# Kernel tuning notes

Measured on AMD Instinct MI355X. Metric: run time of the kernel, lower is better.

Reference implementation:

```python
import jax, jax.numpy as jnp
import numpy as np

B, N, NS, D, HID, MH = 256, 4096, 8, 64, 128, 128
ITERS, EPS, SCALE = 3, 1e-8, D ** -0.5

def _ln(x, g, b):
    m = jnp.mean(x, -1, keepdims=True)
    v = jnp.var(x, -1, keepdims=True)
    return (x - m) * jax.lax.rsqrt(v + 1e-5) * g + b

def _mlp2(x, W1, b1, W2, b2):
    return jax.nn.relu(x @ W1.T + b1) @ W2.T + b2

def _gru(x, h, Wih, Whh, bih, bhh):
    gi = x @ Wih.T + bih
    gh = h @ Whh.T + bhh
    ir, iz, inn = jnp.split(gi, 3, -1)
    hr, hz, hn = jnp.split(gh, 3, -1)
    r = jax.nn.sigmoid(ir + hr)
    z = jax.nn.sigmoid(iz + hz)
    n = jnp.tanh(inn + r * hn)
    return (1 - z) * n + z * h

def _kl(post, prior):
    # KL(N(m_po, exp(lv_po)) || N(m_pr, exp(lv_pr))), diagonal Gaussians, per row
    m_po, lv_po = post[:, :D], post[:, D:]
    m_pr, lv_pr = prior[:, :D], prior[:, D:]
    return 0.5 * jnp.sum(lv_pr - lv_po + (jnp.exp(lv_po) + (m_po - m_pr) ** 2) * jnp.exp(-lv_pr) - 1.0, -1)

def _fwd(inputs, slots, prior_slots, eps_noise, ni_g, ni_b, npf_g, npf_b, Wq, bq, Wk, bk, Wv, bv, sr_W1, sr_b1, sr_W2, sr_b2, pr_W1, pr_b1, pr_W2, pr_b2, gru_Wih, gru_Whh, gru_bih, gru_bhh, mlp_W1, mlp_b1, mlp_W2, mlp_b2):
    b = inputs.shape[0]
    x = _ln(inputs, ni_g, ni_b)               # [b,n,d]
    k = x @ Wk.T + bk
    v = x @ Wv.T + bv
    prior = _mlp2(jax.lax.stop_gradient(prior_slots).reshape(-1, D), pr_W1, pr_b1, pr_W2, pr_b2)  # [b*ns,2d]
    sms = _mlp2(slots.reshape(-1, D), sr_W1, sr_b1, sr_W2, sr_b2).reshape(b, NS, 2 * D)
    mu, logvar = sms[:, :, :D], sms[:, :, D:]
    slots = eps_noise * jnp.exp(0.5 * logvar) + mu   # reparameterize
    kl = jnp.zeros((b * NS,), inputs.dtype)
    for _ in range(ITERS):
        slots_prev = slots
        q = slots @ Wq.T + bq
        dots = jnp.einsum('bid,bjd->bij', q, k) * SCALE   # [b,ns,n]
        attn = jax.nn.softmax(dots, axis=1) + EPS          # softmax over SLOTS (dim=1)
        attn = attn / jnp.sum(attn, -1, keepdims=True)     # renormalize over inputs
        updates = jnp.einsum('bjd,bij->bid', v, attn)      # [b,ns,d]
        slots = _gru(updates.reshape(-1, D), slots_prev.reshape(-1, D), gru_Wih, gru_Whh, gru_bih, gru_bhh).reshape(b, NS, D)
        slots = slots + _mlp2(_ln(slots, npf_g, npf_b), mlp_W1, mlp_b1, mlp_W2, mlp_b2)
        post = _mlp2(slots.reshape(-1, D), sr_W1, sr_b1, sr_W2, sr_b2)
        kl = kl + _kl(post, prior)
    return slots, kl

def setup_inputs() -> dict:
    key = jax.random.key(0)
    ks = jax.random.split(key, 16)
    f32 = jnp.float32
    def w(k, shape):
        return (jax.random.normal(k, shape) * 0.02).astype(f32)
    return {
        'inputs': jax.random.normal(ks[0], (B, N, D), f32),
        'slots': jax.random.normal(ks[1], (B, NS, D), f32),
        'prior_slots': jax.random.normal(ks[2], (B, NS, D), f32),
        'eps_noise': jax.random.normal(ks[3], (B, NS, D), f32),
        'ni_g': jnp.ones((D,), f32), 'ni_b': jnp.zeros((D,), f32),
        'npf_g': jnp.ones((D,), f32), 'npf_b': jnp.zeros((D,), f32),
        'Wq': w(ks[4], (D, D)), 'bq': jnp.zeros((D,), f32),
        'Wk': w(ks[5], (D, D)), 'bk': jnp.zeros((D,), f32),
        'Wv': w(ks[6], (D, D)), 'bv': jnp.zeros((D,), f32),
        'sr_W1': w(ks[7], (HID, D)), 'sr_b1': jnp.zeros((HID,), f32),
        'sr_W2': w(ks[8], (2 * D, HID)), 'sr_b2': jnp.zeros((2 * D,), f32),
        'pr_W1': w(ks[9], (HID, D)), 'pr_b1': jnp.zeros((HID,), f32),
        'pr_W2': w(ks[10], (2 * D, HID)), 'pr_b2': jnp.zeros((2 * D,), f32),
        'gru_Wih': w(ks[11], (3 * D, D)), 'gru_Whh': w(ks[12], (3 * D, D)),
        'gru_bih': jnp.zeros((3 * D,), f32), 'gru_bhh': jnp.zeros((3 * D,), f32),
        'mlp_W1': w(ks[13], (MH, D)), 'mlp_b1': jnp.zeros((MH,), f32),
        'mlp_W2': w(ks[14], (D, MH)), 'mlp_b2': jnp.zeros((D,), f32),
    }

def reference(inputs, slots, prior_slots, eps_noise, ni_g, ni_b, npf_g, npf_b, Wq, bq, Wk, bk, Wv, bv, sr_W1, sr_b1, sr_W2, sr_b2, pr_W1, pr_b1, pr_W2, pr_b2, gru_Wih, gru_Whh, gru_bih, gru_bhh, mlp_W1, mlp_b1, mlp_W2, mlp_b2):
    return _fwd(inputs, slots, prior_slots, eps_noise, ni_g, ni_b, npf_g, npf_b, Wq, bq, Wk, bk, Wv, bv, sr_W1, sr_b1, sr_W2, sr_b2, pr_W1, pr_b1, pr_W2, pr_b2, gru_Wih, gru_Whh, gru_bih, gru_bhh, mlp_W1, mlp_b1, mlp_W2, mlp_b2)
```

## Files before the change

### kernel.cpp

```cpp
#include <hip/hip_runtime.h>
#include <cstdint>
#include <cstddef>


#define B_   256
#define N_   4096
#define EPS_   1e-8f
#define SCALE_ 0.125f
#define OUT_SLOTS_ (B_ * 8 * 64)

typedef unsigned short u16;
typedef unsigned int   u32;
typedef short s16x8 __attribute__((ext_vector_type(8)));
typedef float f32x4 __attribute__((ext_vector_type(4)));

__device__ inline float bf2f(u16 u) {
  union { u32 i; float f; } c; c.i = ((u32)u) << 16; return c.f;
}
__device__ inline u16 f2bf(float f) {
  union { u32 i; float f; } c; c.f = f;
  return (u16)((c.i + 0x7fffu + ((c.i >> 16) & 1u)) >> 16);
}
__device__ inline void bf2x2(u32 u, float& lo, float& hi) {
  union { u32 i; float f; } a, b;
  a.i = u << 16; b.i = u & 0xffff0000u;
  lo = a.f; hi = b.f;
}
__device__ inline float wredsum(float v) {
  #pragma unroll
  for (int o = 32; o; o >>= 1) v += __shfl_xor(v, o, 64);
  return v;
}
__device__ inline float dot64(const float* __restrict__ x, const float* __restrict__ w, float a) {
  #pragma unroll
  for (int ec = 0; ec < 16; ec++) {
    float4 xe = ((const float4*)x)[ec]; float4 we = ((const float4*)w)[ec];
    a = fmaf(xe.x, we.x, a); a = fmaf(xe.y, we.y, a);
    a = fmaf(xe.z, we.z, a); a = fmaf(xe.w, we.w, a);
  }
  return a;
}
__device__ inline float dot128(const float* __restrict__ x, const float* __restrict__ w, float a) {
  #pragma unroll
  for (int ec = 0; ec < 32; ec++) {
    float4 xe = ((const float4*)x)[ec]; float4 we = ((const float4*)w)[ec];
    a = fmaf(xe.x, we.x, a); a = fmaf(xe.y, we.y, a);
    a = fmaf(xe.z, we.z, a); a = fmaf(xe.w, we.w, a);
  }
  return a;
}

__global__ __launch_bounds__(256) void k_ln(
    const float* __restrict__ x, const float* __restrict__ gg,
    const float* __restrict__ bb, u16* __restrict__ XH)
{
  const int tid = threadIdx.x;
  const int xc = tid & 3;
  const int rloc = tid >> 2;
  float4 g4[4], b4[4];
  #pragma unroll
  for (int j = 0; j < 4; j++) {
    g4[j] = *(const float4*)(gg + xc * 16 + j * 4);
    b4[j] = *(const float4*)(bb + xc * 16 + j * 4);
  }
  for (size_t base = (size_t)blockIdx.x * 64; base < (size_t)B_ * N_;
       base += (size_t)gridDim.x * 64) {
    const size_t row = base + rloc;
    const float* xr = x + row * 64 + xc * 16;
    float4 xv[4];
    #pragma unroll
    for (int j = 0; j < 4; j++) xv[j] = ((const float4*)xr)[j];
    float s = 0.f;
    #pragma unroll
    for (int j = 0; j < 4; j++) s += xv[j].x + xv[j].y + xv[j].z + xv[j].w;
    s += __shfl_xor(s, 1, 64); s += __shfl_xor(s, 2, 64);
    const float m = s * (1.0f / 64.0f);
    float vs = 0.f;
    #pragma unroll
    for (int j = 0; j < 4; j++) {
      float a0 = xv[j].x - m, a1 = xv[j].y - m, a2 = xv[j].z - m, a3 = xv[j].w - m;
      vs += a0*a0 + a1*a1 + a2*a2 + a3*a3;
    }
    vs += __shfl_xor(vs, 1, 64); vs += __shfl_xor(vs, 2, 64);
    const float rs = rsqrtf(vs * (1.0f / 64.0f) + 1e-5f);
    u32 pk[8];
    #pragma unroll
    for (int j = 0; j < 4; j++) {
      float h0 = (xv[j].x - m) * rs * g4[j].x + b4[j].x;
      float h1 = (xv[j].y - m) * rs * g4[j].y + b4[j].y;
      float h2 = (xv[j].z - m) * rs * g4[j].z + b4[j].z;
      float h3 = (xv[j].w - m) * rs * g4[j].w + b4[j].w;
      pk[j*2+0] = (u32)f2bf(h0) | ((u32)f2bf(h1) << 16);
      pk[j*2+1] = (u32)f2bf(h2) | ((u32)f2bf(h3) << 16);
    }
    u32* dst = (u32*)(XH + row * 64 + xc * 16);
    ((uint4*)dst)[0] = make_uint4(pk[0], pk[1], pk[2], pk[3]);
    ((uint4*)dst)[1] = make_uint4(pk[4], pk[5], pk[6], pk[7]);
  }
}

__global__ __launch_bounds__(256) void k_setup(
    const float* __restrict__ gWih, const float* __restrict__ gbih,
    const float* __restrict__ Wv,   const float* __restrict__ bv,
    const float* __restrict__ Wq,   const float* __restrict__ bq,
    const float* __restrict__ Wk,   const float* __restrict__ bk,
    float* __restrict__ WF, float* __restrict__ bF,
    float* __restrict__ WQKs, float* __restrict__ bQKs,
    float* __restrict__ wcs, float* __restrict__ c0s)
{
  const int gid = blockIdx.x * 256 + threadIdx.x;
  if (gid < 12288) {
    int r = gid >> 6, e = gid & 63;
    float a = 0.f;
    #pragma unroll 8
    for (int d = 0; d < 64; d++) a = fmaf(gWih[r*64+d], Wv[d*64+e], a);
    WF[gid] = a;
  } else if (gid < 16384) {
    int o = gid - 12288; int t = o >> 6, e = o & 63;
    float a = 0.f;
    #pragma unroll 8
    for (int d = 0; d < 64; d++) a = fmaf(Wq[d*64+t], Wk[d*64+e], a);
    WQKs[o] = a * SCALE_;
  } else if (gid < 16576) {
    int r = gid - 16384;
    float a = gbih[r];
    #pragma unroll 8
    for (int d = 0; d < 64; d++) a = fmaf(gWih[r*64+d], bv[d], a);
    bF[r] = a;
  } else if (gid < 16640) {
    int e = gid - 16576;
    float a = 0.f;
    #pragma unroll 8
    for (int d = 0; d < 64; d++) a = fmaf(bq[d], Wk[d*64+e], a);
    bQKs[e] = a * SCALE_;
  } else if (gid < 16704) {
    int t = gid - 16640;
    float a = 0.f;
    #pragma unroll 8
    for (int d = 0; d < 64; d++) a = fmaf(Wq[d*64+t], bk[d], a);
    wcs[t] = a * SCALE_;
  } else if (gid == 16704) {
    float a = 0.f;
    #pragma unroll 8
    for (int d = 0; d < 64; d++) a = fmaf(bq[d], bk[d], a);
    c0s[0] = a * SCALE_;
  }
}

__global__ __launch_bounds__(256) void k_init(
    const float* __restrict__ slots0, const float* __restrict__ prior_slots,
    const float* __restrict__ eps_noise,
    const float* __restrict__ sr_W1, const float* __restrict__ sr_b1,
    const float* __restrict__ sr_W2, const float* __restrict__ sr_b2,
    const float* __restrict__ pr_W1, const float* __restrict__ pr_b1,
    const float* __restrict__ pr_W2, const float* __restrict__ pr_b2,
    const float* __restrict__ WQKs, const float* __restrict__ bQKs,
    const float* __restrict__ wcs, const float* __restrict__ c0s,
    float* __restrict__ SLOTS, float* __restrict__ PRIOR, float* __restrict__ KLb,
    u16* __restrict__ QP, float* __restrict__ Cb)
{
  __shared__ float sl[256], hid[512], pst[512];
  const int tid = threadIdx.x;
  const int w = tid >> 6, lane = tid & 63;
  const int gs0 = blockIdx.x * 4;
  const int b = gs0 >> 3;
  const int gs = gs0 + w;

  sl[tid] = slots0[(size_t)gs0 * 64 + tid];
  #pragma unroll
  for (int kk = 0; kk < 2; kk++) {
    int idx = tid + kk * 256; int sloc = idx >> 7, h = idx & 127;
    float a = dot64(prior_slots + (size_t)(gs0 + sloc) * 64, pr_W1 + h * 64, pr_b1[h]);
    hid[idx] = fmaxf(a, 0.f);
  }
  __syncthreads();
  #pragma unroll
  for (int kk = 0; kk < 2; kk++) {
    int idx = tid + kk * 256; int sloc = idx >> 7, o = idx & 127;
    PRIOR[(size_t)(gs0 + sloc) * 128 + o] =
        dot128(hid + sloc * 128, pr_W2 + o * 128, pr_b2[o]);
  }
  __syncthreads();
  #pragma unroll
  for (int kk = 0; kk < 2; kk++) {
    int idx = tid + kk * 256; int sloc = idx >> 7, h = idx & 127;
    float a = dot64(sl + sloc * 64, sr_W1 + h * 64, sr_b1[h]);
    hid[idx] = fmaxf(a, 0.f);
  }
  __syncthreads();
  #pragma unroll
  for (int kk = 0; kk < 2; kk++) {
    int idx = tid + kk * 256; int sloc = idx >> 7, o = idx & 127;
    pst[idx] = dot128(hid + sloc * 128, sr_W2 + o * 128, sr_b2[o]);
  }
  __syncthreads();
  {
    float mu = pst[w * 128 + lane];
    float lv = pst[w * 128 + 64 + lane];
    float sv = eps_noise[(size_t)gs * 64 + lane] * __expf(0.5f * lv) + mu;
    sl[tid] = sv;
    SLOTS[(size_t)gs * 64 + lane] = sv;
  }
  __syncthreads();
  {
    float a = bQKs[lane];
    #pragma unroll 8
    for (int t2 = 0; t2 < 64; t2++) a = fmaf(sl[w * 64 + t2], WQKs[t2 * 64 + lane], a);
    QP[(size_t)b * 1024 + (gs & 7) * 64 + lane] = f2bf(a);
    float part = wredsum(sl[tid] * wcs[lane]);
    if (lane == 0) { Cb[b * 16 + (gs & 7)] = part + c0s[0]; KLb[gs] = 0.f; }
    QP[(size_t)b * 1024 + 512 + (blockIdx.x & 1) * 256 + tid] = 0;
    if ((blockIdx.x & 1) == 0 && tid < 8) Cb[b * 16 + 8 + tid] = 0.f;
  }
}

__global__ __launch_bounds__(256, 4) void k_attn(
    const u16* __restrict__ XH, const u16* __restrict__ QP,
    const float* __restrict__ Cb,
    float* __restrict__ Upart, float* __restrict__ Spart)
{
  __shared__ float attn[8][516];
  __shared__ float updw[4][512];
  __shared__ float sS[4][8];
  const int tid  = threadIdx.x;
  const int lane = tid & 63, wv = tid >> 6;
  const int col  = lane & 15, kg = lane >> 4;
  const int bc   = blockIdx.x;
  const int b    = bc >> 3;
  const u16* Xb = XH + (size_t)bc * 512 * 64;

  union { uint4 q; s16x8 v; } a0, a1;
  const u16* qr = QP + (size_t)b * 1024 + col * 64 + kg * 8;
  a0.q = *(const uint4*)(qr);
  a1.q = *(const uint4*)(qr + 32);
  float4 cv = *(const float4*)(Cb + b * 16 + kg * 4);

  const int jb = wv * 128;
  float s_loc[4] = {0.f, 0.f, 0.f, 0.f};
  union { uint4 q; s16x8 v; } b0, b1, n0, n1;
  {
    const u16* kp = Xb + (size_t)(jb + col) * 64 + kg * 8;
    b0.q = *(const uint4*)kp; b1.q = *(const uint4*)(kp + 32);
  }
  #pragma unroll 1
  for (int t = 0; t < 8; t++) {
    const u16* kn = Xb + (size_t)(jb + (((t + 1) & 7) << 4) + col) * 64 + kg * 8;
    n0.q = *(const uint4*)kn; n1.q = *(const uint4*)(kn + 32);
    f32x4 acc = {0.f, 0.f, 0.f, 0.f};
    acc = __builtin_amdgcn_mfma_f32_16x16x32_bf16(a0.v, b0.v, acc, 0, 0, 0);
    acc = __builtin_amdgcn_mfma_f32_16x16x32_bf16(a1.v, b1.v, acc, 0, 0, 0);
    float d0 = acc[0] + cv.x, d1 = acc[1] + cv.y;
    float d2 = acc[2] + cv.z, d3 = acc[3] + cv.w;
    float m4 = fmaxf(fmaxf(d0, d1), fmaxf(d2, d3));
    float m8 = fmaxf(m4, __shfl_xor(m4, 16, 64));
    float e0 = __expf(d0 - m8), e1 = __expf(d1 - m8);
    float e2 = __expf(d2 - m8), e3 = __expf(d3 - m8);
    float s4 = e0 + e1 + e2 + e3;
    float s8 = s4 + __shfl_xor(s4, 16, 64);
    float rinv = 1.0f / s8;
    float v0 = fmaf(e0, rinv, EPS_), v1 = fmaf(e1, rinv, EPS_);
    float v2 = fmaf(e2, rinv, EPS_), v3 = fmaf(e3, rinv, EPS_);
    if (kg < 2) {
      int j = jb + t * 16 + col;
      attn[kg*4+0][j] = v0; attn[kg*4+1][j] = v1;
      attn[kg*4+2][j] = v2; attn[kg*4+3][j] = v3;
      s_loc[0] += v0; s_loc[1] += v1; s_loc[2] += v2; s_loc[3] += v3;
    }
    b0 = n0; b1 = n1;
  }
  #pragma unroll
  for (int r = 0; r < 4; r++) {
    #pragma unroll
    for (int o = 1; o < 16; o <<= 1) s_loc[r] += __shfl_xor(s_loc[r], o, 64);
  }
  if (kg < 2 && col == 0) {
    #pragma unroll
    for (int r = 0; r < 4; r++) sS[wv][kg * 4 + r] = s_loc[r];
  }

  const int pxo  = lane >> 4;
  const int dimc = lane & 15;
  float u[8][4];
  #pragma unroll
  for (int i = 0; i < 8; i++)
    #pragma unroll
    for (int dd = 0; dd < 4; dd++) u[i][dd] = 0.f;
  #pragma unroll 4
  for (int jg = 0; jg < 32; jg++) {
    int j = jb + jg * 4 + pxo;
    uint2 xv2 = *(const uint2*)(Xb + (size_t)j * 64 + dimc * 4);
    float x0, x1, x2, x3;
    bf2x2(xv2.x, x0, x1); bf2x2(xv2.y, x2, x3);
    #pragma unroll
    for (int i = 0; i < 8; i++) {
      float a = attn[i][j];
      u[i][0] = fmaf(a, x0, u[i][0]); u[i][1] = fmaf(a, x1, u[i][1]);
      u[i][2] = fmaf(a, x2, u[i][2]); u[i][3] = fmaf(a, x3, u[i][3]);
    }
  }
  #pragma unroll
  for (int i = 0; i < 8; i++)
    #pragma unroll
    for (int dd = 0; dd < 4; dd++) {
      u[i][dd] += __shfl_xor(u[i][dd], 16, 64);
      u[i][dd] += __shfl_xor(u[i][dd], 32, 64);
    }
  if (lane < 16) {
    #pragma unroll
    for (int i = 0; i < 8; i++)
      #pragma unroll
      for (int dd = 0; dd < 4; dd++)
        updw[wv][i * 64 + lane * 4 + dd] = u[i][dd];
  }
  __syncthreads();
  #pragma unroll
  for (int k2 = 0; k2 < 2; k2++) {
    int idx = tid + k2 * 256;
    Upart[(size_t)bc * 512 + idx] =
        updw[0][idx] + updw[1][idx] + updw[2][idx] + updw[3][idx];
  }
  if (tid < 8)
    Spart[bc * 8 + tid] = sS[0][tid] + sS[1][tid] + sS[2][tid] + sS[3][tid];
}

__global__ __launch_bounds__(256) void k_update(
    float* __restrict__ SLOTS, const float* __restrict__ Upart,
    const float* __restrict__ Spart, const float* __restrict__ PRIOR,
    float* __restrict__ KLb, u16* __restrict__ QP, float* __restrict__ Cb,
    const float* __restrict__ npf_g, const float* __restrict__ npf_b,
    const float* __restrict__ WF, const float* __restrict__ bF,
    const float* __restrict__ gWhh, const float* __restrict__ gbhh,
    const float* __restrict__ WQKs, const float* __restrict__ bQKs,
    const float* __restrict__ wcs, const float* __restrict__ c0s,
    const float* __restrict__ sr_W1, const float* __restrict__ sr_b1,
    const float* __restrict__ sr_W2, const float* __restrict__ sr_b2,
    const float* __restrict__ mW1, const float* __restrict__ mb1,
    const float* __restrict__ mW2, const float* __restrict__ mb2,
    float* __restrict__ out, int last)
{
  __shared__ float uav[256], spl[256], sl[256], lnb[256], hid[512], pst[512];
  const int tid = threadIdx.x;
  const int w = tid >> 6, lane = tid & 63;
  const int gs = blockIdx.x * 4 + w;
  const int b = gs >> 3, s = gs & 7;

  {
    const float* up = Upart + (size_t)b * 4096 + s * 64 + lane;
    float usum = 0.f;
    #pragma unroll
    for (int c = 0; c < 8; c++) usum += up[c * 512];
    const float* sp2 = Spart + b * 64 + s;
    float Sv = 0.f;
    #pragma unroll
    for (int c = 0; c < 8; c++) Sv += sp2[c * 8];
    uav[tid] = usum * (1.0f / Sv);
    spl[tid] = SLOTS[(size_t)gs * 64 + lane];
  }
  __syncthreads();
  {
    const float* ur = uav + w * 64;
    const float* hr = spl + w * 64;
    const float* wi0 = WF + lane * 64;
    const float* wi1 = WF + (64 + lane) * 64;
    const float* wi2 = WF + (128 + lane) * 64;
    const float* wh0 = gWhh + lane * 64;
    const float* wh1 = gWhh + (64 + lane) * 64;
    const float* wh2 = gWhh + (128 + lane) * 64;
    float air = 0.f, aiz = 0.f, ain = 0.f, ahr = 0.f, ahz = 0.f, ahn = 0.f;
    #pragma unroll
    for (int ec = 0; ec < 16; ec++) {
      float4 xe = ((const float4*)ur)[ec];
      float4 he = ((const float4*)hr)[ec];
      float4 ww;
      ww = ((const float4*)wi0)[ec];
      air = fmaf(xe.x,ww.x,air); air = fmaf(xe.y,ww.y,air);
      air = fmaf(xe.z,ww.z,air); air = fmaf(xe.w,ww.w,air);
      ww = ((const float4*)wi1)[ec];
      aiz = fmaf(xe.x,ww.x,aiz); aiz = fmaf(xe.y,ww.y,aiz);
      aiz = fmaf(xe.z,ww.z,aiz); aiz = fmaf(xe.w,ww.w,aiz);
      ww = ((const float4*)wi2)[ec];
      ain = fmaf(xe.x,ww.x,ain); ain = fmaf(xe.y,ww.y,ain);
      ain = fmaf(xe.z,ww.z,ain); ain = fmaf(xe.w,ww.w,ain);
      ww = ((const float4*)wh0)[ec];
      ahr = fmaf(he.x,ww.x,ahr); ahr = fmaf(he.y,ww.y,ahr);
      ahr = fmaf(he.z,ww.z,ahr); ahr = fmaf(he.w,ww.w,ahr);
      ww = ((const float4*)wh1)[ec];
      ahz = fmaf(he.x,ww.x,ahz); ahz = fmaf(he.y,ww.y,ahz);
      ahz = fmaf(he.z,ww.z,ahz); ahz = fmaf(he.w,ww.w,ahz);
      ww = ((const float4*)wh2)[ec];
      ahn = fmaf(he.x,ww.x,ahn); ahn = fmaf(he.y,ww.y,ahn);
      ahn = fmaf(he.z,ww.z,ahn); ahn = fmaf(he.w,ww.w,ahn);
    }
    float rr = 1.0f / (1.0f + __expf(-(air + bF[lane]       + ahr + gbhh[lane])));
    float zz = 1.0f / (1.0f + __expf(-(aiz + bF[64 + lane]  + ahz + gbhh[64 + lane])));
    float nn = tanhf(ain + bF[128 + lane] + rr * (ahn + gbhh[128 + lane]));
    float hnew = (1.0f - zz) * nn + zz * spl[tid];
    sl[tid] = hnew;
    float mm = wredsum(hnew) * (1.0f / 64.0f);
    float cc = hnew - mm;
    float va = wredsum(cc * cc) * (1.0f / 64.0f);
    lnb[tid] = cc * rsqrtf(va + 1e-5f) * npf_g[lane] + npf_b[lane];
  }
  __syncthreads();
  #pragma unroll
  for (int kk = 0; kk < 2; kk++) {
    int idx = tid + kk * 256; int sloc = idx >> 7, h = idx & 127;
    float a = dot64(lnb + sloc * 64, mW1 + h * 64, mb1[h]);
    hid[idx] = fmaxf(a, 0.f);
  }
  __syncthreads();
  sl[tid] += dot128(hid + w * 128, mW2 + lane * 128, mb2[lane]);
  __syncthreads();
  #pragma unroll
  for (int kk = 0; kk < 2; kk++) {
    int idx = tid + kk * 256; int sloc = idx >> 7, h = idx & 127;
    float a = dot64(sl + sloc * 64, sr_W1 + h * 64, sr_b1[h]);
    hid[idx] = fmaxf(a, 0.f);
  }
  __syncthreads();
  #pragma unroll
  for (int kk = 0; kk < 2; kk++) {
    int idx = tid + kk * 256; int sloc = idx >> 7, o = idx & 127;
    pst[idx] = dot128(hid + sloc * 128, sr_W2 + o * 128, sr_b2[o]);
  }
  __syncthreads();
  {
    float m_po = pst[w * 128 + lane],  lv_po = pst[w * 128 + 64 + lane];
    float m_pr = PRIOR[(size_t)gs * 128 + lane];
    float lv_pr = PRIOR[(size_t)gs * 128 + 64 + lane];
    float dm = m_po - m_pr;
    float term = lv_pr - lv_po + (__expf(lv_po) + dm * dm) * __expf(-lv_pr) - 1.0f;
    float tsum = wredsum(term);
    if (lane == 0) {
      float k2 = KLb[gs] + 0.5f * tsum;
      KLb[gs] = k2;
      if (last) out[OUT_SLOTS_ + gs] = k2;
    }
    if (last) {
      out[(size_t)gs * 64 + lane] = sl[tid];
    } else {
      SLOTS[(size_t)gs * 64 + lane] = sl[tid];
      float a = bQKs[lane];
      #pragma unroll 8
      for (int t2 = 0; t2 < 64; t2++) a = fmaf(sl[w * 64 + t2], WQKs[t2 * 64 + lane], a);
      QP[(size_t)b * 1024 + s * 64 + lane] = f2bf(a);
      float part = wredsum(sl[tid] * wcs[lane]);
      if (lane == 0) Cb[b * 16 + s] = part + c0s[0];
    }
  }
}

extern "C" void kernel_launch(void* const* d_in, const int* in_sizes, int n_in,
                              void* d_out, int out_size, void* d_ws, size_t ws_size,
                              hipStream_t stream) {
  (void)in_sizes; (void)n_in; (void)out_size; (void)ws_size;
  const float* inputs      = (const float*)d_in[0];
  const float* slots0      = (const float*)d_in[1];
  const float* prior_slots = (const float*)d_in[2];
  const float* eps_noise   = (const float*)d_in[3];
  const float* ni_g  = (const float*)d_in[4];
  const float* ni_b  = (const float*)d_in[5];
  const float* npf_g = (const float*)d_in[6];
  const float* npf_b = (const float*)d_in[7];
  const float* Wq = (const float*)d_in[8];   const float* bq = (const float*)d_in[9];
  const float* Wk = (const float*)d_in[10];  const float* bk = (const float*)d_in[11];
  const float* Wv = (const float*)d_in[12];  const float* bv = (const float*)d_in[13];
  const float* sr_W1 = (const float*)d_in[14]; const float* sr_b1 = (const float*)d_in[15];
  const float* sr_W2 = (const float*)d_in[16]; const float* sr_b2 = (const float*)d_in[17];
  const float* pr_W1 = (const float*)d_in[18]; const float* pr_b1 = (const float*)d_in[19];
  const float* pr_W2 = (const float*)d_in[20]; const float* pr_b2 = (const float*)d_in[21];
  const float* gWih = (const float*)d_in[22]; const float* gWhh = (const float*)d_in[23];
  const float* gbih = (const float*)d_in[24]; const float* gbhh = (const float*)d_in[25];
  const float* mW1 = (const float*)d_in[26]; const float* mb1 = (const float*)d_in[27];
  const float* mW2 = (const float*)d_in[28]; const float* mb2 = (const float*)d_in[29];

  char* ws = (char*)d_ws;
  u16*   XH    = (u16*)  (ws);
  float* Upart = (float*)(ws + 134217728);
  float* Spart = (float*)(ws + 138412032);
  u16*   QP    = (u16*)  (ws + 138477568);
  float* Cb    = (float*)(ws + 139001856);
  float* SLOTS = (float*)(ws + 139018240);
  float* PRIOR = (float*)(ws + 139542528);
  float* KLb   = (float*)(ws + 140591104);
  float* WF    = (float*)(ws + 140599296);
  float* WQKs  = (float*)(ws + 140648448);
  float* bF    = (float*)(ws + 140664832);
  float* bQKs  = (float*)(ws + 140665600);
  float* wcs   = (float*)(ws + 140665856);
  float* c0s   = (float*)(ws + 140666112);

  k_setup<<<dim3(66), dim3(256), 0, stream>>>(
      gWih, gbih, Wv, bv, Wq, bq, Wk, bk, WF, bF, WQKs, bQKs, wcs, c0s);
  k_ln<<<dim3(4096), dim3(256), 0, stream>>>(inputs, ni_g, ni_b, XH);
  k_init<<<dim3(512), dim3(256), 0, stream>>>(
      slots0, prior_slots, eps_noise,
      sr_W1, sr_b1, sr_W2, sr_b2, pr_W1, pr_b1, pr_W2, pr_b2,
      WQKs, bQKs, wcs, c0s, SLOTS, PRIOR, KLb, QP, Cb);
  for (int it = 0; it < 3; it++) {
    k_attn<<<dim3(2048), dim3(256), 0, stream>>>(XH, QP, Cb, Upart, Spart);
    k_update<<<dim3(512), dim3(256), 0, stream>>>(
        SLOTS, Upart, Spart, PRIOR, KLb, QP, Cb,
        npf_g, npf_b, WF, bF, gWhh, gbhh, WQKs, bQKs, wcs, c0s,
        sr_W1, sr_b1, sr_W2, sr_b2, mW1, mb1, mW2, mb2,
        (float*)d_out, it == 2);
  }
}
```

Baseline: 768.2 us.

## Fuse setup kernels into one launch and use MFMA for attention-value product

Merges the layernorm, weight-precompute and slot-init kernels into a single launch partitioned by block index. The init path now computes q explicitly and projects it through Wk instead of reading precomputed WQKs, so it no longer depends on the fused precompute blocks. In the attention kernel, the scalar FMA loop that multiplied attention weights by bf16 inputs is replaced with bf16 MFMA: attention weights and input tiles are staged through LDS per 32-pixel group. The update kernel switches to per-wave LDS slices and redistributes MLP work per wave. The MFMA path rounds attention weights to bf16, adds per-group block syncs and uses strided LDS reads for the B operand.

```diff
diff --git a/kernel.cpp b/kernel.cpp
--- a/kernel.cpp
+++ b/kernel.cpp
@@ -14,17 +14,9 @@
 typedef short s16x8 __attribute__((ext_vector_type(8)));
 typedef float f32x4 __attribute__((ext_vector_type(4)));
 
-__device__ inline float bf2f(u16 u) {
-  union { u32 i; float f; } c; c.i = ((u32)u) << 16; return c.f;
-}
 __device__ inline u16 f2bf(float f) {
   union { u32 i; float f; } c; c.f = f;
   return (u16)((c.i + 0x7fffu + ((c.i >> 16) & 1u)) >> 16);
-}
-__device__ inline void bf2x2(u32 u, float& lo, float& hi) {
-  union { u32 i; float f; } a, b;
-  a.i = u << 16; b.i = u & 0xffff0000u;
-  lo = a.f; hi = b.f;
 }
 __device__ inline float wredsum(float v) {
   #pragma unroll
@@ -50,167 +42,150 @@
   return a;
 }
 
-__global__ __launch_bounds__(256) void k_ln(
+__global__ __launch_bounds__(256) void k_pre(
     const float* __restrict__ x, const float* __restrict__ gg,
-    const float* __restrict__ bb, u16* __restrict__ XH)
-{
-  const int tid = threadIdx.x;
-  const int xc = tid & 3;
-  const int rloc = tid >> 2;
-  float4 g4[4], b4[4];
-  #pragma unroll
-  for (int j = 0; j < 4; j++) {
-    g4[j] = *(const float4*)(gg + xc * 16 + j * 4);
-    b4[j] = *(const float4*)(bb + xc * 16 + j * 4);
-  }
-  for (size_t base = (size_t)blockIdx.x * 64; base < (size_t)B_ * N_;
-       base += (size_t)gridDim.x * 64) {
-    const size_t row = base + rloc;
-    const float* xr = x + row * 64 + xc * 16;
-    float4 xv[4];
-    #pragma unroll
-    for (int j = 0; j < 4; j++) xv[j] = ((const float4*)xr)[j];
-    float s = 0.f;
-    #pragma unroll
-    for (int j = 0; j < 4; j++) s += xv[j].x + xv[j].y + xv[j].z + xv[j].w;
-    s += __shfl_xor(s, 1, 64); s += __shfl_xor(s, 2, 64);
-    const float m = s * (1.0f / 64.0f);
-    float vs = 0.f;
-    #pragma unroll
-    for (int j = 0; j < 4; j++) {
-      float a0 = xv[j].x - m, a1 = xv[j].y - m, a2 = xv[j].z - m, a3 = xv[j].w - m;
-      vs += a0*a0 + a1*a1 + a2*a2 + a3*a3;
-    }
-    vs += __shfl_xor(vs, 1, 64); vs += __shfl_xor(vs, 2, 64);
-    const float rs = rsqrtf(vs * (1.0f / 64.0f) + 1e-5f);
-    u32 pk[8];
-    #pragma unroll
-    for (int j = 0; j < 4; j++) {
-      float h0 = (xv[j].x - m) * rs * g4[j].x + b4[j].x;
-      float h1 = (xv[j].y - m) * rs * g4[j].y + b4[j].y;
-      float h2 = (xv[j].z - m) * rs * g4[j].z + b4[j].z;
-      float h3 = (xv[j].w - m) * rs * g4[j].w + b4[j].w;
-      pk[j*2+0] = (u32)f2bf(h0) | ((u32)f2bf(h1) << 16);
-      pk[j*2+1] = (u32)f2bf(h2) | ((u32)f2bf(h3) << 16);
-    }
-    u32* dst = (u32*)(XH + row * 64 + xc * 16);
-    ((uint4*)dst)[0] = make_uint4(pk[0], pk[1], pk[2], pk[3]);
-    ((uint4*)dst)[1] = make_uint4(pk[4], pk[5], pk[6], pk[7]);
-  }
-}
-
-__global__ __launch_bounds__(256) void k_setup(
-    const float* __restrict__ gWih, const float* __restrict__ gbih,
-    const float* __restrict__ Wv,   const float* __restrict__ bv,
-    const float* __restrict__ Wq,   const float* __restrict__ bq,
-    const float* __restrict__ Wk,   const float* __restrict__ bk,
-    float* __restrict__ WF, float* __restrict__ bF,
-    float* __restrict__ WQKs, float* __restrict__ bQKs,
-    float* __restrict__ wcs, float* __restrict__ c0s)
-{
-  const int gid = blockIdx.x * 256 + threadIdx.x;
-  if (gid < 12288) {
-    int r = gid >> 6, e = gid & 63;
-    float a = 0.f;
-    #pragma unroll 8
-    for (int d = 0; d < 64; d++) a = fmaf(gWih[r*64+d], Wv[d*64+e], a);
-    WF[gid] = a;
-  } else if (gid < 16384) {
-    int o = gid - 12288; int t = o >> 6, e = o & 63;
-    float a = 0.f;
-    #pragma unroll 8
-    for (int d = 0; d < 64; d++) a = fmaf(Wq[d*64+t], Wk[d*64+e], a);
-    WQKs[o] = a * SCALE_;
-  } else if (gid < 16576) {
-    int r = gid - 16384;
-    float a = gbih[r];
-    #pragma unroll 8
-    for (int d = 0; d < 64; d++) a = fmaf(gWih[r*64+d], bv[d], a);
-    bF[r] = a;
-  } else if (gid < 16640) {
-    int e = gid - 16576;
-    float a = 0.f;
-    #pragma unroll 8
-    for (int d = 0; d < 64; d++) a = fmaf(bq[d], Wk[d*64+e], a);
-    bQKs[e] = a * SCALE_;
-  } else if (gid < 16704) {
-    int t = gid - 16640;
-    float a = 0.f;
-    #pragma unroll 8
-    for (int d = 0; d < 64; d++) a = fmaf(Wq[d*64+t], bk[d], a);
-    wcs[t] = a * SCALE_;
-  } else if (gid == 16704) {
-    float a = 0.f;
-    #pragma unroll 8
-    for (int d = 0; d < 64; d++) a = fmaf(bq[d], bk[d], a);
-    c0s[0] = a * SCALE_;
-  }
-}
-
-__global__ __launch_bounds__(256) void k_init(
+    const float* __restrict__ bb, u16* __restrict__ XH,
     const float* __restrict__ slots0, const float* __restrict__ prior_slots,
     const float* __restrict__ eps_noise,
     const float* __restrict__ sr_W1, const float* __restrict__ sr_b1,
     const float* __restrict__ sr_W2, const float* __restrict__ sr_b2,
     const float* __restrict__ pr_W1, const float* __restrict__ pr_b1,
     const float* __restrict__ pr_W2, const float* __restrict__ pr_b2,
-    const float* __restrict__ WQKs, const float* __restrict__ bQKs,
-    const float* __restrict__ wcs, const float* __restrict__ c0s,
+    const float* __restrict__ Wq,   const float* __restrict__ bq,
+    const float* __restrict__ Wk,   const float* __restrict__ bk,
+    const float* __restrict__ gWih, const float* __restrict__ gbih,
+    const float* __restrict__ Wv,   const float* __restrict__ bv,
     float* __restrict__ SLOTS, float* __restrict__ PRIOR, float* __restrict__ KLb,
-    u16* __restrict__ QP, float* __restrict__ Cb)
+    u16* __restrict__ QP, float* __restrict__ Cb,
+    float* __restrict__ WF, float* __restrict__ bF,
+    float* __restrict__ WQKs, float* __restrict__ bQKs,
+    float* __restrict__ wcs, float* __restrict__ c0s)
 {
-  __shared__ float sl[256], hid[512], pst[512];
+  __shared__ float ism[4][256];
   const int tid = threadIdx.x;
-  const int w = tid >> 6, lane = tid & 63;
-  const int gs0 = blockIdx.x * 4;
-  const int b = gs0 >> 3;
-  const int gs = gs0 + w;
-
-  sl[tid] = slots0[(size_t)gs0 * 64 + tid];
-  #pragma unroll
-  for (int kk = 0; kk < 2; kk++) {
-    int idx = tid + kk * 256; int sloc = idx >> 7, h = idx & 127;
-    float a = dot64(prior_slots + (size_t)(gs0 + sloc) * 64, pr_W1 + h * 64, pr_b1[h]);
-    hid[idx] = fmaxf(a, 0.f);
-  }
-  __syncthreads();
-  #pragma unroll
-  for (int kk = 0; kk < 2; kk++) {
-    int idx = tid + kk * 256; int sloc = idx >> 7, o = idx & 127;
-    PRIOR[(size_t)(gs0 + sloc) * 128 + o] =
-        dot128(hid + sloc * 128, pr_W2 + o * 128, pr_b2[o]);
-  }
-  __syncthreads();
-  #pragma unroll
-  for (int kk = 0; kk < 2; kk++) {
-    int idx = tid + kk * 256; int sloc = idx >> 7, h = idx & 127;
-    float a = dot64(sl + sloc * 64, sr_W1 + h * 64, sr_b1[h]);
-    hid[idx] = fmaxf(a, 0.f);
-  }
-  __syncthreads();
-  #pragma unroll
-  for (int kk = 0; kk < 2; kk++) {
-    int idx = tid + kk * 256; int sloc = idx >> 7, o = idx & 127;
-    pst[idx] = dot128(hid + sloc * 128, sr_W2 + o * 128, sr_b2[o]);
-  }
-  __syncthreads();
-  {
-    float mu = pst[w * 128 + lane];
-    float lv = pst[w * 128 + 64 + lane];
+  const int bid = blockIdx.x;
+
+  if (bid < 4096) {
+    const int xc = tid & 3;
+    const int rloc = tid >> 2;
+    float4 g4[4], b4[4];
+    #pragma unroll
+    for (int j = 0; j < 4; j++) {
+      g4[j] = *(const float4*)(gg + xc * 16 + j * 4);
+      b4[j] = *(const float4*)(bb + xc * 16 + j * 4);
+    }
+    for (int it = 0; it < 4; it++) {
+      const size_t row = ((size_t)bid + (size_t)it * 4096) * 64 + rloc;
+      const float* xr = x + row * 64 + xc * 16;
+      float4 xv[4];
+      #pragma unroll
+      for (int j = 0; j < 4; j++) xv[j] = ((const float4*)xr)[j];
+      float s = 0.f;
+      #pragma unroll
+      for (int j = 0; j < 4; j++) s += xv[j].x + xv[j].y + xv[j].z + xv[j].w;
+      s += __shfl_xor(s, 1, 64); s += __shfl_xor(s, 2, 64);
+      const float m = s * (1.0f / 64.0f);
+      float vs = 0.f;
+      #pragma unroll
+      for (int j = 0; j < 4; j++) {
+        float a0 = xv[j].x - m, a1 = xv[j].y - m, a2 = xv[j].z - m, a3 = xv[j].w - m;
+        vs += a0*a0 + a1*a1 + a2*a2 + a3*a3;
+      }
+      vs += __shfl_xor(vs, 1, 64); vs += __shfl_xor(vs, 2, 64);
+      const float rs = rsqrtf(vs * (1.0f / 64.0f) + 1e-5f);
+      u32 pk[8];
+      #pragma unroll
+      for (int j = 0; j < 4; j++) {
+        float h0 = (xv[j].x - m) * rs * g4[j].x + b4[j].x;
+        float h1 = (xv[j].y - m) * rs * g4[j].y + b4[j].y;
+        float h2 = (xv[j].z - m) * rs * g4[j].z + b4[j].z;
+        float h3 = (xv[j].w - m) * rs * g4[j].w + b4[j].w;
+        pk[j*2+0] = (u32)f2bf(h0) | ((u32)f2bf(h1) << 16);
+        pk[j*2+1] = (u32)f2bf(h2) | ((u32)f2bf(h3) << 16);
+      }
+      u32* dst = (u32*)(XH + row * 64 + xc * 16);
+      ((uint4*)dst)[0] = make_uint4(pk[0], pk[1], pk[2], pk[3]);
+      ((uint4*)dst)[1] = make_uint4(pk[4], pk[5], pk[6], pk[7]);
+    }
+  } else if (bid < 4608) {
+    const int ib = bid - 4096;
+    const int w = tid >> 6, lane = tid & 63;
+    const int gs = ib * 4 + w;
+    const int b  = gs >> 3;
+    float* slL  = ism[w];
+    float* hidL = ism[w] + 64;
+    float* qL   = ism[w] + 192;
+
+    slL[lane] = slots0[(size_t)gs * 64 + lane];
+    const float* prow = prior_slots + (size_t)gs * 64;
+    float ph0 = dot64(prow, pr_W1 + lane * 64,        pr_b1[lane]);
+    float ph1 = dot64(prow, pr_W1 + (64 + lane) * 64, pr_b1[64 + lane]);
+    hidL[lane]      = fmaxf(ph0, 0.f);
+    hidL[64 + lane] = fmaxf(ph1, 0.f);
+    __syncthreads();
+    PRIOR[(size_t)gs * 128 + lane]      = dot128(hidL, pr_W2 + lane * 128,        pr_b2[lane]);
+    PRIOR[(size_t)gs * 128 + 64 + lane] = dot128(hidL, pr_W2 + (64 + lane) * 128, pr_b2[64 + lane]);
+    __syncthreads();
+    float sh0 = dot64(slL, sr_W1 + lane * 64,        sr_b1[lane]);
+    float sh1 = dot64(slL, sr_W1 + (64 + lane) * 64, sr_b1[64 + lane]);
+    hidL[lane]      = fmaxf(sh0, 0.f);
+    hidL[64 + lane] = fmaxf(sh1, 0.f);
+    __syncthreads();
+    float mu = dot128(hidL, sr_W2 + lane * 128,        sr_b2[lane]);
+    float lv = dot128(hidL, sr_W2 + (64 + lane) * 128, sr_b2[64 + lane]);
     float sv = eps_noise[(size_t)gs * 64 + lane] * __expf(0.5f * lv) + mu;
-    sl[tid] = sv;
     SLOTS[(size_t)gs * 64 + lane] = sv;
-  }
-  __syncthreads();
-  {
-    float a = bQKs[lane];
+    slL[lane] = sv;
+    __syncthreads();
+    float q = dot64(slL, Wq + lane * 64, bq[lane]);
+    qL[lane] = q;
+    __syncthreads();
+    float qp = 0.f;
     #pragma unroll 8
-    for (int t2 = 0; t2 < 64; t2++) a = fmaf(sl[w * 64 + t2], WQKs[t2 * 64 + lane], a);
-    QP[(size_t)b * 1024 + (gs & 7) * 64 + lane] = f2bf(a);
-    float part = wredsum(sl[tid] * wcs[lane]);
-    if (lane == 0) { Cb[b * 16 + (gs & 7)] = part + c0s[0]; KLb[gs] = 0.f; }
-    QP[(size_t)b * 1024 + 512 + (blockIdx.x & 1) * 256 + tid] = 0;
-    if ((blockIdx.x & 1) == 0 && tid < 8) Cb[b * 16 + 8 + tid] = 0.f;
+    for (int t2 = 0; t2 < 64; t2++) qp = fmaf(qL[t2], Wk[t2 * 64 + lane], qp);
+    QP[(size_t)b * 1024 + (gs & 7) * 64 + lane] = f2bf(qp * SCALE_);
+    float c = wredsum(q * bk[lane]) * SCALE_;
+    if (lane == 0) { Cb[b * 16 + (gs & 7)] = c; KLb[gs] = 0.f; }
+    QP[(size_t)b * 1024 + 512 + (ib & 1) * 256 + tid] = 0;
+    if ((ib & 1) == 0 && tid < 8) Cb[b * 16 + 8 + tid] = 0.f;
+  } else {
+    const int gid = (bid - 4608) * 256 + tid;
+    if (gid < 12288) {
+      int r = gid >> 6, e = gid & 63;
+      float a = 0.f;
+      #pragma unroll 8
+      for (int d = 0; d < 64; d++) a = fmaf(gWih[r*64+d], Wv[d*64+e], a);
+      WF[gid] = a;
+    } else if (gid < 16384) {
+      int o = gid - 12288; int t = o >> 6, e = o & 63;
+      float a = 0.f;
+      #pragma unroll 8
+      for (int d = 0; d < 64; d++) a = fmaf(Wq[d*64+t], Wk[d*64+e], a);
+      WQKs[o] = a * SCALE_;
+    } else if (gid < 16576) {
+      int r = gid - 16384;
+      float a = gbih[r];
+      #pragma unroll 8
+      for (int d = 0; d < 64; d++) a = fmaf(gWih[r*64+d], bv[d], a);
+      bF[r] = a;
+    } else if (gid < 16640) {
+      int e = gid - 16576;
+      float a = 0.f;
+      #pragma unroll 8
+      for (int d = 0; d < 64; d++) a = fmaf(bq[d], Wk[d*64+e], a);
+      bQKs[e] = a * SCALE_;
+    } else if (gid < 16704) {
+      int t = gid - 16640;
+      float a = 0.f;
+      #pragma unroll 8
+      for (int d = 0; d < 64; d++) a = fmaf(Wq[d*64+t], bk[d], a);
+      wcs[t] = a * SCALE_;
+    } else if (gid == 16704) {
+      float a = 0.f;
+      #pragma unroll 8
+      for (int d = 0; d < 64; d++) a = fmaf(bq[d], bk[d], a);
+      c0s[0] = a * SCALE_;
+    }
   }
 }
 
@@ -219,7 +194,8 @@
     const float* __restrict__ Cb,
     float* __restrict__ Upart, float* __restrict__ Spart)
 {
-  __shared__ float attn[8][516];
+  __shared__ u16   xls[4][32 * 66];
+  __shared__ u16   atbs[4][16 * 32];
   __shared__ float updw[4][512];
   __shared__ float sS[4][8];
   const int tid  = threadIdx.x;
@@ -228,6 +204,13 @@
   const int bc   = blockIdx.x;
   const int b    = bc >> 3;
   const u16* Xb = XH + (size_t)bc * 512 * 64;
+  u16* xlw = xls[wv];
+  u16* atw = atbs[wv];
+
+  {
+    u32* az = (u32*)(atw + 8 * 32);
+    az[lane] = 0; az[64 + lane] = 0;
+  }
 
   union { uint4 q; s16x8 v; } a0, a1;
   const u16* qr = QP + (size_t)b * 1024 + col * 64 + kg * 8;
@@ -237,37 +220,67 @@
 
   const int jb = wv * 128;
   float s_loc[4] = {0.f, 0.f, 0.f, 0.f};
-  union { uint4 q; s16x8 v; } b0, b1, n0, n1;
-  {
-    const u16* kp = Xb + (size_t)(jb + col) * 64 + kg * 8;
-    b0.q = *(const uint4*)kp; b1.q = *(const uint4*)(kp + 32);
-  }
+  f32x4 uac[4];
+  #pragma unroll
+  for (int dt = 0; dt < 4; dt++) uac[dt] = (f32x4){0.f, 0.f, 0.f, 0.f};
+
   #pragma unroll 1
-  for (int t = 0; t < 8; t++) {
-    const u16* kn = Xb + (size_t)(jb + (((t + 1) & 7) << 4) + col) * 64 + kg * 8;
-    n0.q = *(const uint4*)kn; n1.q = *(const uint4*)(kn + 32);
-    f32x4 acc = {0.f, 0.f, 0.f, 0.f};
-    acc = __builtin_amdgcn_mfma_f32_16x16x32_bf16(a0.v, b0.v, acc, 0, 0, 0);
-    acc = __builtin_amdgcn_mfma_f32_16x16x32_bf16(a1.v, b1.v, acc, 0, 0, 0);
-    float d0 = acc[0] + cv.x, d1 = acc[1] + cv.y;
-    float d2 = acc[2] + cv.z, d3 = acc[3] + cv.w;
-    float m4 = fmaxf(fmaxf(d0, d1), fmaxf(d2, d3));
-    float m8 = fmaxf(m4, __shfl_xor(m4, 16, 64));
-    float e0 = __expf(d0 - m8), e1 = __expf(d1 - m8);
-    float e2 = __expf(d2 - m8), e3 = __expf(d3 - m8);
-    float s4 = e0 + e1 + e2 + e3;
-    float s8 = s4 + __shfl_xor(s4, 16, 64);
-    float rinv = 1.0f / s8;
-    float v0 = fmaf(e0, rinv, EPS_), v1 = fmaf(e1, rinv, EPS_);
-    float v2 = fmaf(e2, rinv, EPS_), v3 = fmaf(e3, rinv, EPS_);
-    if (kg < 2) {
-      int j = jb + t * 16 + col;
-      attn[kg*4+0][j] = v0; attn[kg*4+1][j] = v1;
-      attn[kg*4+2][j] = v2; attn[kg*4+3][j] = v3;
-      s_loc[0] += v0; s_loc[1] += v1; s_loc[2] += v2; s_loc[3] += v3;
-    }
-    b0 = n0; b1 = n1;
-  }
+  for (int g = 0; g < 4; g++) {
+    const u16* kp0 = Xb + (size_t)(jb + g * 32 + col) * 64 + kg * 8;
+    const u16* kp1 = Xb + (size_t)(jb + g * 32 + 16 + col) * 64 + kg * 8;
+    union { uint4 q; s16x8 v; } b0, b1, b2, b3;
+    b0.q = *(const uint4*)(kp0); b1.q = *(const uint4*)(kp0 + 32);
+    b2.q = *(const uint4*)(kp1); b3.q = *(const uint4*)(kp1 + 32);
+
+    #pragma unroll
+    for (int e = 0; e < 2; e++) {
+      const s16x8 fb0 = e ? b2.v : b0.v;
+      const s16x8 fb1 = e ? b3.v : b1.v;
+      f32x4 acc = {0.f, 0.f, 0.f, 0.f};
+      acc = __builtin_amdgcn_mfma_f32_16x16x32_bf16(a0.v, fb0, acc, 0, 0, 0);
+      acc = __builtin_amdgcn_mfma_f32_16x16x32_bf16(a1.v, fb1, acc, 0, 0, 0);
+      float d0 = acc[0] + cv.x, d1 = acc[1] + cv.y;
+      float d2 = acc[2] + cv.z, d3 = acc[3] + cv.w;
+      float m4 = fmaxf(fmaxf(d0, d1), fmaxf(d2, d3));
+      float m8 = fmaxf(m4, __shfl_xor(m4, 16, 64));
+      float e0 = __expf(d0 - m8), e1 = __expf(d1 - m8);
+      float e2 = __expf(d2 - m8), e3 = __expf(d3 - m8);
+      float s4 = e0 + e1 + e2 + e3;
+      float s8 = s4 + __shfl_xor(s4, 16, 64);
+      float rinv = 1.0f / s8;
+      float v0 = fmaf(e0, rinv, EPS_), v1 = fmaf(e1, rinv, EPS_);
+      float v2 = fmaf(e2, rinv, EPS_), v3 = fmaf(e3, rinv, EPS_);
+      const int pxg = e * 16 + col;
+      {
+        u32* xw0 = (u32*)(xlw + pxg * 66 + kg * 8);
+        u32* xw1 = (u32*)(xlw + pxg * 66 + 32 + kg * 8);
+        union { uint4 q; } t0, t1;
+        t0.q = e ? b2.q : b0.q; t1.q = e ? b3.q : b1.q;
+        xw0[0] = t0.q.x; xw0[1] = t0.q.y; xw0[2] = t0.q.z; xw0[3] = t0.q.w;
+        xw1[0] = t1.q.x; xw1[1] = t1.q.y; xw1[2] = t1.q.z; xw1[3] = t1.q.w;
+      }
+      if (kg < 2) {
+        atw[(kg * 4 + 0) * 32 + pxg] = f2bf(v0);
+        atw[(kg * 4 + 1) * 32 + pxg] = f2bf(v1);
+        atw[(kg * 4 + 2) * 32 + pxg] = f2bf(v2);
+        atw[(kg * 4 + 3) * 32 + pxg] = f2bf(v3);
+        s_loc[0] += v0; s_loc[1] += v1; s_loc[2] += v2; s_loc[3] += v3;
+      }
+    }
+    __syncthreads();
+    union { uint4 q; s16x8 v; } af;
+    af.q = *(const uint4*)(atw + col * 32 + kg * 8);
+    #pragma unroll
+    for (int dt = 0; dt < 4; dt++) {
+      union { s16x8 v; u16 u[8]; } bf;
+      #pragma unroll
+      for (int tt = 0; tt < 8; tt++)
+        bf.u[tt] = xlw[(kg * 8 + tt) * 66 + dt * 16 + col];
+      uac[dt] = __builtin_amdgcn_mfma_f32_16x16x32_bf16(af.v, bf.v, uac[dt], 0, 0, 0);
+    }
+    __syncthreads();
+  }
+
   #pragma unroll
   for (int r = 0; r < 4; r++) {
     #pragma unroll
@@ -277,40 +290,12 @@
     #pragma unroll
     for (int r = 0; r < 4; r++) sS[wv][kg * 4 + r] = s_loc[r];
   }
-
-  const int pxo  = lane >> 4;
-  const int dimc = lane & 15;
-  float u[8][4];
-  #pragma unroll
-  for (int i = 0; i < 8; i++)
-    #pragma unroll
-    for (int dd = 0; dd < 4; dd++) u[i][dd] = 0.f;
-  #pragma unroll 4
-  for (int jg = 0; jg < 32; jg++) {
-    int j = jb + jg * 4 + pxo;
-    uint2 xv2 = *(const uint2*)(Xb + (size_t)j * 64 + dimc * 4);
-    float x0, x1, x2, x3;
-    bf2x2(xv2.x, x0, x1); bf2x2(xv2.y, x2, x3);
-    #pragma unroll
-    for (int i = 0; i < 8; i++) {
-      float a = attn[i][j];
-      u[i][0] = fmaf(a, x0, u[i][0]); u[i][1] = fmaf(a, x1, u[i][1]);
-      u[i][2] = fmaf(a, x2, u[i][2]); u[i][3] = fmaf(a, x3, u[i][3]);
-    }
-  }
-  #pragma unroll
-  for (int i = 0; i < 8; i++)
-    #pragma unroll
-    for (int dd = 0; dd < 4; dd++) {
-      u[i][dd] += __shfl_xor(u[i][dd], 16, 64);
-      u[i][dd] += __shfl_xor(u[i][dd], 32, 64);
-    }
-  if (lane < 16) {
-    #pragma unroll
-    for (int i = 0; i < 8; i++)
-      #pragma unroll
-      for (int dd = 0; dd < 4; dd++)
-        updw[wv][i * 64 + lane * 4 + dd] = u[i][dd];
+  if (kg < 2) {
+    #pragma unroll
+    for (int dt = 0; dt < 4; dt++)
+      #pragma unroll
+      for (int r = 0; r < 4; r++)
+        updw[wv][(kg * 4 + r) * 64 + dt * 16 + col] = uac[dt][r];
   }
   __syncthreads();
   #pragma unroll
@@ -338,11 +323,16 @@
     const float* __restrict__ mW2, const float* __restrict__ mb2,
     float* __restrict__ out, int last)
 {
-  __shared__ float uav[256], spl[256], sl[256], lnb[256], hid[512], pst[512];
+  __shared__ float ism[4][448];
   const int tid = threadIdx.x;
   const int w = tid >> 6, lane = tid & 63;
   const int gs = blockIdx.x * 4 + w;
   const int b = gs >> 3, s = gs & 7;
+  float* uavL = ism[w];
+  float* splL = ism[w] + 64;
+  float* lnbL = ism[w] + 128;
+  float* hidL = ism[w] + 192;
+  float* slL  = ism[w] + 320;
 
   {
     const float* up = Upart + (size_t)b * 4096 + s * 64 + lane;
@@ -353,13 +343,14 @@
     float Sv = 0.f;
     #pragma unroll
     for (int c = 0; c < 8; c++) Sv += sp2[c * 8];
-    uav[tid] = usum * (1.0f / Sv);
-    spl[tid] = SLOTS[(size_t)gs * 64 + lane];
-  }
-  __syncthreads();
+    uavL[lane] = usum * (1.0f / Sv);
+    splL[lane] = SLOTS[(size_t)gs * 64 + lane];
+  }
+  __syncthreads();
+  float hnew;
   {
-    const float* ur = uav + w * 64;
-    const float* hr = spl + w * 64;
+    const float* ur = uavL;
+    const float* hr = splL;
     const float* wi0 = WF + lane * 64;
     const float* wi1 = WF + (64 + lane) * 64;
     const float* wi2 = WF + (128 + lane) * 64;
@@ -394,39 +385,26 @@
     float rr = 1.0f / (1.0f + __expf(-(air + bF[lane]       + ahr + gbhh[lane])));
     float zz = 1.0f / (1.0f + __expf(-(aiz + bF[64 + lane]  + ahz + gbhh[64 + lane])));
     float nn = tanhf(ain + bF[128 + lane] + rr * (ahn + gbhh[128 + lane]));
-    float hnew = (1.0f - zz) * nn + zz * spl[tid];
-    sl[tid] = hnew;
+    hnew = (1.0f - zz) * nn + zz * splL[lane];
     float mm = wredsum(hnew) * (1.0f / 64.0f);
     float cc = hnew - mm;
     float va = wredsum(cc * cc) * (1.0f / 64.0f);
-    lnb[tid] = cc * rsqrtf(va + 1e-5f) * npf_g[lane] + npf_b[lane];
-  }
-  __syncthreads();
-  #pragma unroll
-  for (int kk = 0; kk < 2; kk++) {
-    int idx = tid + kk * 256; int sloc = idx >> 7, h = idx & 127;
-    float a = dot64(lnb + sloc * 64, mW1 + h * 64, mb1[h]);
-    hid[idx] = fmaxf(a, 0.f);
-  }
-  __syncthreads();
-  sl[tid] += dot128(hid + w * 128, mW2 + lane * 128, mb2[lane]);
-  __syncthreads();
-  #pragma unroll
-  for (int kk = 0; kk < 2; kk++) {
-    int idx = tid + kk * 256; int sloc = idx >> 7, h = idx & 127;
-    float a = dot64(sl + sloc * 64, sr_W1 + h * 64, sr_b1[h]);
-    hid[idx] = fmaxf(a, 0.f);
-  }
-  __syncthreads();
-  #pragma unroll
-  for (int kk = 0; kk < 2; kk++) {
-    int idx = tid + kk * 256; int sloc = idx >> 7, o = idx & 127;
-    pst[idx] = dot128(hid + sloc * 128, sr_W2 + o * 128, sr_b2[o]);
-  }
-  __syncthreads();
+    lnbL[lane] = cc * rsqrtf(va + 1e-5f) * npf_g[lane] + npf_b[lane];
+  }
+  __syncthreads();
+  hidL[lane]      = fmaxf(dot64(lnbL, mW1 + lane * 64,        mb1[lane]), 0.f);
+  hidL[64 + lane] = fmaxf(dot64(lnbL, mW1 + (64 + lane) * 64, mb1[64 + lane]), 0.f);
+  __syncthreads();
+  float sl = hnew + dot128(hidL, mW2 + lane * 128, mb2[lane]);
+  slL[lane] = sl;
+  __syncthreads();
+  hidL[lane]      = fmaxf(dot64(slL, sr_W1 + lane * 64,        sr_b1[lane]), 0.f);
+  hidL[64 + lane] = fmaxf(dot64(slL, sr_W1 + (64 + lane) * 64, sr_b1[64 + lane]), 0.f);
+  __syncthreads();
+  float m_po  = dot128(hidL, sr_W2 + lane * 128,        sr_b2[lane]);
+  float lv_po = dot128(hidL, sr_W2 + (64 + lane) * 128, sr_b2[64 + lane]);
   {
-    float m_po = pst[w * 128 + lane],  lv_po = pst[w * 128 + 64 + lane];
-    float m_pr = PRIOR[(size_t)gs * 128 + lane];
+    float m_pr  = PRIOR[(size_t)gs * 128 + lane];
     float lv_pr = PRIOR[(size_t)gs * 128 + 64 + lane];
     float dm = m_po - m_pr;
     float term = lv_pr - lv_po + (__expf(lv_po) + dm * dm) * __expf(-lv_pr) - 1.0f;
@@ -437,14 +415,14 @@
       if (last) out[OUT_SLOTS_ + gs] = k2;
     }
     if (last) {
-      out[(size_t)gs * 64 + lane] = sl[tid];
+      out[(size_t)gs * 64 + lane] = sl;
     } else {
-      SLOTS[(size_t)gs * 64 + lane] = sl[tid];
+      SLOTS[(size_t)gs * 64 + lane] = sl;
       float a = bQKs[lane];
       #pragma unroll 8
-      for (int t2 = 0; t2 < 64; t2++) a = fmaf(sl[w * 64 + t2], WQKs[t2 * 64 + lane], a);
+      for (int t2 = 0; t2 < 64; t2++) a = fmaf(slL[t2], WQKs[t2 * 64 + lane], a);
       QP[(size_t)b * 1024 + s * 64 + lane] = f2bf(a);
-      float part = wredsum(sl[tid] * wcs[lane]);
+      float part = wredsum(sl * wcs[lane]);
       if (lane == 0) Cb[b * 16 + s] = part + c0s[0];
     }
   }
@@ -490,13 +468,13 @@
   float* wcs   = (float*)(ws + 140665856);
   float* c0s   = (float*)(ws + 140666112);
 
-  k_setup<<<dim3(66), dim3(256), 0, stream>>>(
-      gWih, gbih, Wv, bv, Wq, bq, Wk, bk, WF, bF, WQKs, bQKs, wcs, c0s);
-  k_ln<<<dim3(4096), dim3(256), 0, stream>>>(inputs, ni_g, ni_b, XH);
-  k_init<<<dim3(512), dim3(256), 0, stream>>>(
+  k_pre<<<dim3(4674), dim3(256), 0, stream>>>(
+      inputs, ni_g, ni_b, XH,
       slots0, prior_slots, eps_noise,
       sr_W1, sr_b1, sr_W2, sr_b2, pr_W1, pr_b1, pr_W2, pr_b2,
-      WQKs, bQKs, wcs, c0s, SLOTS, PRIOR, KLb, QP, Cb);
+      Wq, bq, Wk, bk, gWih, gbih, Wv, bv,
+      SLOTS, PRIOR, KLb, QP, Cb,
+      WF, bF, WQKs, bQKs, wcs, c0s);
   for (int it = 0; it < 3; it++) {
     k_attn<<<dim3(2048), dim3(256), 0, stream>>>(XH, QP, Cb, Upart, Spart);
     k_update<<<dim3(512), dim3(256), 0, stream>>>(
```

Result: no change. 772.1 us (+0.5%).
